# Kernel tuning notes

Hardware: AMD Instinct MI355X
Metric: run time of the kernel (lower is better)

## Reference

```python
import jax, jax.numpy as jnp
from jax import lax
import numpy as np

UNITS = 400
FEAT = 3
B, T = 64, 512


def _lstm_layer(x, Wx, Wh, pi, pf, po, b):
    """Peephole LSTM (Graves 2013). x: [B,T,D] -> [B,T,U]."""
    Bsz = x.shape[0]
    U = Wh.shape[0]
    # Precompute input projections for all timesteps: [B,T,4U]
    xproj = jnp.einsum('btd,dk->btk', x, Wx) + b
    xs = jnp.swapaxes(xproj, 0, 1)  # [T,B,4U]

    def step(carry, xp):
        h, c = carry
        z = xp + h @ Wh  # [B,4U]
        zi, zf, zg, zo = jnp.split(z, 4, axis=-1)
        i = jax.nn.sigmoid(zi + pi * c)
        f = jax.nn.sigmoid(zf + pf * c)
        g = jnp.tanh(zg)
        c_new = f * c + i * g
        o = jax.nn.sigmoid(zo + po * c_new)
        h_new = o * jnp.tanh(c_new)
        return (h_new, c_new), h_new

    init = (jnp.zeros((Bsz, U), x.dtype), jnp.zeros((Bsz, U), x.dtype))
    _, hs = lax.scan(step, init, xs)
    return jnp.swapaxes(hs, 0, 1)  # [B,T,U]


def setup_inputs() -> dict:
    key = jax.random.key(0)
    ks = jax.random.split(key, 32)
    ki = iter(range(32))
    s = 0.05
    d = {'x': jax.random.normal(ks[next(ki)], (B, T, FEAT), jnp.float32)}
    in_dims = [FEAT, UNITS, UNITS]
    for l, din in enumerate(in_dims):
        d[f'Wx{l}'] = jax.random.normal(ks[next(ki)], (din, 4 * UNITS), jnp.float32) * s
        d[f'Wh{l}'] = jax.random.normal(ks[next(ki)], (UNITS, 4 * UNITS), jnp.float32) * s
        d[f'pi{l}'] = jax.random.normal(ks[next(ki)], (UNITS,), jnp.float32) * s
        d[f'pf{l}'] = jax.random.normal(ks[next(ki)], (UNITS,), jnp.float32) * s
        d[f'po{l}'] = jax.random.normal(ks[next(ki)], (UNITS,), jnp.float32) * s
        d[f'b{l}'] = jnp.zeros((4 * UNITS,), jnp.float32)
    d['Wd'] = jax.random.normal(ks[next(ki)], (UNITS, FEAT), jnp.float32) * s
    d['bd'] = jnp.zeros((FEAT,), jnp.float32)
    return d


def reference(x, Wx0, Wh0, pi0, pf0, po0, b0,
              Wx1, Wh1, pi1, pf1, po1, b1,
              Wx2, Wh2, pi2, pf2, po2, b2,
              Wd, bd):
    h = _lstm_layer(x, Wx0, Wh0, pi0, pf0, po0, b0)
    h = _lstm_layer(h, Wx1, Wh1, pi1, pf1, po1, b1)
    h = _lstm_layer(h, Wx2, Wh2, pi2, pf2, po2, b2)
    return h @ Wd + bd  # [B,T,FEAT]
```

## Files before the change

### kernel.cpp

```cpp
#include <hip/hip_runtime.h>
#include <math.h>

#define B64   64
#define TT    512
#define U400  400
#define G1600 1600
#define NBPL  80
#define UPB   5
#define NCOL  (4 * UPB)
#define NW    8
#define NTHR  512
#define NBLK  (3 * NBPL)

__device__ __forceinline__ float ldg_c(const float* p) {
  return __hip_atomic_load(p, __ATOMIC_RELAXED, __HIP_MEMORY_SCOPE_AGENT);
}
__device__ __forceinline__ void stg_c(float* p, float v) {
  __hip_atomic_store(p, v, __ATOMIC_RELAXED, __HIP_MEMORY_SCOPE_AGENT);
}
__device__ __forceinline__ int adl(const unsigned* p) {
  return (int)__hip_atomic_load(p, __ATOMIC_RELAXED, __HIP_MEMORY_SCOPE_AGENT);
}

__global__ void xpose_x_k(const float* __restrict__ x, float* __restrict__ xT) {
  int idx = blockIdx.x * 256 + threadIdx.x;
  if (idx < B64 * TT * 3) {
    int d = idx % 3;
    int t = (idx / 3) % TT;
    int b = idx / (3 * TT);
    xT[(t * 3 + d) * B64 + b] = x[idx];
  }
}

__global__ void transpose_k(const float* __restrict__ in, float* __restrict__ out,
                            int R, int C) {
  __shared__ float tile[32][33];
  int bx = blockIdx.x * 32, by = blockIdx.y * 32;
  int tx = threadIdx.x, ty = threadIdx.y;
  #pragma unroll
  for (int i = ty; i < 32; i += 8) {
    int r = by + i, c = bx + tx;
    if (r < R && c < C) tile[i][tx] = in[(size_t)r * C + c];
  }
  __syncthreads();
  #pragma unroll
  for (int i = ty; i < 32; i += 8) {
    int r = bx + i, c = by + tx;
    if (r < C && c < R) out[(size_t)r * R + c] = tile[tx][i];
  }
}

template <int NQ>
__device__ __forceinline__ void gemm_q(const float* __restrict__ aslab,
                                       int lane,
                                       const float* __restrict__ wg0,
                                       const float* __restrict__ wg1,
                                       const float* __restrict__ wg2,
                                       const float* __restrict__ wg3,
                                       float (&acc)[NCOL]) {
  #pragma unroll 4
  for (int q = 0; q < NQ; ++q) {
    const float a0 = ldg_c(aslab + (size_t)(4 * q + 0) * B64 + lane);
    const float a1 = ldg_c(aslab + (size_t)(4 * q + 1) * B64 + lane);
    const float a2 = ldg_c(aslab + (size_t)(4 * q + 2) * B64 + lane);
    const float a3 = ldg_c(aslab + (size_t)(4 * q + 3) * B64 + lane);
    #pragma unroll
    for (int uu = 0; uu < UPB; ++uu) {
      const float4 w = *reinterpret_cast<const float4*>(wg0 + uu * U400 + 4 * q);
      acc[0 * UPB + uu] += a0 * w.x + a1 * w.y + a2 * w.z + a3 * w.w;
    }
    #pragma unroll
    for (int uu = 0; uu < UPB; ++uu) {
      const float4 w = *reinterpret_cast<const float4*>(wg1 + uu * U400 + 4 * q);
      acc[1 * UPB + uu] += a0 * w.x + a1 * w.y + a2 * w.z + a3 * w.w;
    }
    #pragma unroll
    for (int uu = 0; uu < UPB; ++uu) {
      const float4 w = *reinterpret_cast<const float4*>(wg2 + uu * U400 + 4 * q);
      acc[2 * UPB + uu] += a0 * w.x + a1 * w.y + a2 * w.z + a3 * w.w;
    }
    #pragma unroll
    for (int uu = 0; uu < UPB; ++uu) {
      const float4 w = *reinterpret_cast<const float4*>(wg3 + uu * U400 + 4 * q);
      acc[3 * UPB + uu] += a0 * w.x + a1 * w.y + a2 * w.z + a3 * w.w;
    }
  }
}

struct ScanP {
  const float *xT0, *Wx0;
  const float *WxT1, *WxT2;
  const float *WhT0, *WhT1, *WhT2;
  const float *b0, *b1, *b2;
  const float *pi0, *pi1, *pi2;
  const float *pf0, *pf1, *pf2;
  const float *po0, *po1, *po2;
  float *h0r, *h1r;
  float *h2;
  unsigned *sync;
};

__launch_bounds__(NTHR, 1)
__global__ void lstm_scan_k(ScanP p) {
  const int l    = blockIdx.x / NBPL;
  const int u0   = (blockIdx.x % NBPL) * UPB;
  const int lane = threadIdx.x & 63;
  const int kq   = __builtin_amdgcn_readfirstlane(threadIdx.x >> 6);

  __shared__ float zs[NW][NCOL][B64];

  const float* WhT  = (l == 0) ? p.WhT0 : (l == 1 ? p.WhT1 : p.WhT2);
  const float* WxT  = (l == 1) ? p.WxT1 : p.WxT2;
  const float* bias = (l == 0) ? p.b0  : (l == 1 ? p.b1  : p.b2);
  const float* pi   = (l == 0) ? p.pi0 : (l == 1 ? p.pi1 : p.pi2);
  const float* pf   = (l == 0) ? p.pf0 : (l == 1 ? p.pf1 : p.pf2);
  const float* po   = (l == 0) ? p.po0 : (l == 1 ? p.po1 : p.po2);
  const float* prevb = (l == 1) ? p.h0r : p.h1r;
  float* ownb = (l == 0) ? p.h0r : (l == 1 ? p.h1r : p.h2);
  const int ownmask = (l == 2) ? (TT - 1) : 7;

  unsigned* cnt  = p.sync;
  unsigned* acc_ = p.sync + 3;

  const float* wb; int k0, isH;
  if (l == 0) {
    wb = WhT; isH = 1;
    k0 = (kq < 4) ? kq * 52 : 208 + (kq - 4) * 48;
  } else if (kq < 4) {
    wb = WxT; isH = 0; k0 = kq * 100;
  } else {
    wb = WhT; isH = 1; k0 = (kq - 4) * 100;
  }

  const float* wg0 = wb + (size_t)(0 * U400 + u0) * U400 + k0;
  const float* wg1 = wb + (size_t)(1 * U400 + u0) * U400 + k0;
  const float* wg2 = wb + (size_t)(2 * U400 + u0) * U400 + k0;
  const float* wg3 = wb + (size_t)(3 * U400 + u0) * U400 + k0;

  float creg = 0.f;

  for (int t = 0; t < TT; ++t) {
    if (threadIdx.x == 0) {
      while (adl(&cnt[l]) < t) __builtin_amdgcn_s_sleep(1);
      if (l > 0)
        while (adl(&cnt[l - 1]) < t + 1) __builtin_amdgcn_s_sleep(1);
      if (l < 2)
        while (adl(&cnt[l + 1]) < t - 7) __builtin_amdgcn_s_sleep(1);
    }
    __syncthreads();

    {
      float acc[NCOL];
      #pragma unroll
      for (int c = 0; c < NCOL; ++c) acc[c] = 0.f;

      if (!(isH && t == 0)) {
        const float* aslab = isH
            ? ownb  + (size_t)((t - 1) & ownmask) * (U400 * B64) + (size_t)k0 * B64
            : prevb + (size_t)(t & 7)             * (U400 * B64) + (size_t)k0 * B64;
        if (l == 0) {
          if (kq < 4) gemm_q<13>(aslab, lane, wg0, wg1, wg2, wg3, acc);
          else        gemm_q<12>(aslab, lane, wg0, wg1, wg2, wg3, acc);
        } else {
          gemm_q<25>(aslab, lane, wg0, wg1, wg2, wg3, acc);
        }
      }
      #pragma unroll
      for (int c = 0; c < NCOL; ++c) zs[kq][c][lane] = acc[c];
    }
    __syncthreads();

    if (threadIdx.x < UPB * B64) {
      const int uu = threadIdx.x >> 6;
      const int b  = lane;
      const int u  = u0 + uu;
      float z0 = bias[0 * U400 + u], z1 = bias[1 * U400 + u];
      float z2 = bias[2 * U400 + u], z3 = bias[3 * U400 + u];
      #pragma unroll
      for (int w = 0; w < NW; ++w) {
        z0 += zs[w][0 * UPB + uu][b];
        z1 += zs[w][1 * UPB + uu][b];
        z2 += zs[w][2 * UPB + uu][b];
        z3 += zs[w][3 * UPB + uu][b];
      }
      if (l == 0) {
        #pragma unroll
        for (int dd = 0; dd < 3; ++dd) {
          float xv = p.xT0[(t * 3 + dd) * B64 + b];
          z0 += xv * p.Wx0[dd * G1600 + 0 * U400 + u];
          z1 += xv * p.Wx0[dd * G1600 + 1 * U400 + u];
          z2 += xv * p.Wx0[dd * G1600 + 2 * U400 + u];
          z3 += xv * p.Wx0[dd * G1600 + 3 * U400 + u];
        }
      }
      float cp = creg;
      float ig = 1.f / (1.f + expf(-(z0 + pi[u] * cp)));
      float fg = 1.f / (1.f + expf(-(z1 + pf[u] * cp)));
      float gg = tanhf(z2);
      float cn = fg * cp + ig * gg;
      float og = 1.f / (1.f + expf(-(z3 + po[u] * cn)));
      creg = cn;
      float h = og * tanhf(cn);
      stg_c(&ownb[(size_t)(t & ownmask) * (U400 * B64) + (size_t)u * B64 + b], h);
    }

    __syncthreads();

    if (threadIdx.x == 0) {
      unsigned old = __hip_atomic_fetch_add(&acc_[l], 1u, __ATOMIC_RELAXED,
                                            __HIP_MEMORY_SCOPE_AGENT);
      if (old == (unsigned)((t + 1) * NBPL - 1))
        __hip_atomic_store(&cnt[l], (unsigned)(t + 1), __ATOMIC_RELAXED,
                           __HIP_MEMORY_SCOPE_AGENT);
    }
  }
}

__launch_bounds__(256)
__global__ void dense_k(const float* __restrict__ h2, const float* __restrict__ Wd,
                        const float* __restrict__ bd, float* __restrict__ out) {
  int wid  = blockIdx.x * 4 + (threadIdx.x >> 6);
  int lane = threadIdx.x & 63;
  int t = wid / 3, f = wid - t * 3;
  if (t >= TT) return;
  float acc = bd[f];
  const float* hrow = h2 + (size_t)t * U400 * B64 + lane;
  #pragma unroll 4
  for (int u = 0; u < U400; ++u) acc += hrow[(size_t)u * B64] * Wd[u * 3 + f];
  out[((size_t)lane * TT + t) * 3 + f] = acc;
}

extern "C" void kernel_launch(void* const* d_in, const int* in_sizes, int n_in,
                              void* d_out, int out_size, void* d_ws, size_t ws_size,
                              hipStream_t stream) {
  const float* x   = (const float*)d_in[0];
  const float* Wx0 = (const float*)d_in[1];
  const float* Wh0 = (const float*)d_in[2];
  const float* pi0 = (const float*)d_in[3];
  const float* pf0 = (const float*)d_in[4];
  const float* po0 = (const float*)d_in[5];
  const float* b0  = (const float*)d_in[6];
  const float* Wx1 = (const float*)d_in[7];
  const float* Wh1 = (const float*)d_in[8];
  const float* pi1 = (const float*)d_in[9];
  const float* pf1 = (const float*)d_in[10];
  const float* po1 = (const float*)d_in[11];
  const float* b1  = (const float*)d_in[12];
  const float* Wx2 = (const float*)d_in[13];
  const float* Wh2 = (const float*)d_in[14];
  const float* pi2 = (const float*)d_in[15];
  const float* pf2 = (const float*)d_in[16];
  const float* po2 = (const float*)d_in[17];
  const float* b2  = (const float*)d_in[18];
  const float* Wd  = (const float*)d_in[19];
  const float* bd  = (const float*)d_in[20];

  float* ws   = (float*)d_ws;
  float* xT0  = ws;
  float* WhT0 = xT0  + 98304;
  float* WhT1 = WhT0 + 640000;
  float* WhT2 = WhT1 + 640000;
  float* WxT1 = WhT2 + 640000;
  float* WxT2 = WxT1 + 640000;
  float* h0r  = WxT2 + 640000;
  float* h1r  = h0r  + 204800;
  float* h2   = h1r  + 204800;
  unsigned* syn = (unsigned*)(h2 + 13107200);

  hipMemsetAsync(syn, 0, 64, stream);

  hipLaunchKernelGGL(xpose_x_k, dim3(384), dim3(256), 0, stream, x, xT0);

  dim3 tb(32, 8);
  dim3 tg((G1600 + 31) / 32, (U400 + 31) / 32);
  hipLaunchKernelGGL(transpose_k, tg, tb, 0, stream, Wh0, WhT0, U400, G1600);
  hipLaunchKernelGGL(transpose_k, tg, tb, 0, stream, Wh1, WhT1, U400, G1600);
  hipLaunchKernelGGL(transpose_k, tg, tb, 0, stream, Wh2, WhT2, U400, G1600);
  hipLaunchKernelGGL(transpose_k, tg, tb, 0, stream, Wx1, WxT1, U400, G1600);
  hipLaunchKernelGGL(transpose_k, tg, tb, 0, stream, Wx2, WxT2, U400, G1600);

  ScanP hp;
  hp.xT0 = xT0;  hp.Wx0 = Wx0;
  hp.WxT1 = WxT1; hp.WxT2 = WxT2;
  hp.WhT0 = WhT0; hp.WhT1 = WhT1; hp.WhT2 = WhT2;
  hp.b0 = b0; hp.b1 = b1; hp.b2 = b2;
  hp.pi0 = pi0; hp.pi1 = pi1; hp.pi2 = pi2;
  hp.pf0 = pf0; hp.pf1 = pf1; hp.pf2 = pf2;
  hp.po0 = po0; hp.po1 = po1; hp.po2 = po2;
  hp.h0r = h0r; hp.h1r = h1r; hp.h2 = h2;
  hp.sync = syn;

  void* args[] = { &hp };
  hipLaunchCooperativeKernel((void*)lstm_scan_k, dim3(NBLK), dim3(NTHR),
                             args, 0, stream);

  hipLaunchKernelGGL(dense_k, dim3(384), dim3(256), 0, stream, h2, Wd, bd,
                     (float*)d_out);
}
```

Before: 21.50 ms.

## Split input-projection GEMMs into separate producer blocks and fuse dense head into scan

Layers 1 and 2 previously had each block compute both the Wx·h_prev and Wh·h_self products inside the recurrent critical path. Dedicated blocks now compute the input projections into ring buffers ahead of time, so the recurrent blocks only do the Wh GEMM over all 400 k and add precomputed values. Blocks per layer go from 80 to 50 with 8 units each. The dense output layer becomes one extra block that consumes h2 from an 8-deep ring buffer, which removes the full h2 buffer and the separate kernel launch. Sync counters are padded onto separate cache lines, and a new backpressure edge from the dense block gates layer 2. The cost is more blocks, more inter-block dependencies and an extra global round trip for the projections.

```diff
diff --git a/kernel.cpp b/kernel.cpp
--- a/kernel.cpp
+++ b/kernel.cpp
@@ -5,12 +5,14 @@
 #define TT    512
 #define U400  400
 #define G1600 1600
-#define NBPL  80
-#define UPB   5
+#define NBPL  50
+#define UPB   8
 #define NCOL  (4 * UPB)
 #define NW    8
 #define NTHR  512
-#define NBLK  (3 * NBPL)
+#define NBWH  (3 * NBPL)
+#define NBWX  (2 * NBPL)
+#define NBLK  (NBWH + NBWX + 1)
 
 __device__ __forceinline__ float ldg_c(const float* p) {
   return __hip_atomic_load(p, __ATOMIC_RELAXED, __HIP_MEMORY_SCOPE_AGENT);
@@ -95,42 +97,79 @@
   const float *pi0, *pi1, *pi2;
   const float *pf0, *pf1, *pf2;
   const float *po0, *po1, *po2;
-  float *h0r, *h1r;
-  float *h2;
-  unsigned *sync;
+  const float *Wd, *bd;
+  float *h0r, *h1r, *h2r;
+  float *zx1, *zx2;
+  float *outp;
+  unsigned *syn;
 };
 
-__launch_bounds__(NTHR, 1)
+#define CNT(l)  (p.syn + (l) * 32)
+#define XCNT(l) (p.syn + (3 + (l)) * 32)
+#define DCNT    (p.syn + 6 * 32)
+#define AAC(l)  (p.syn + (7 + (l)) * 32)
+#define XAC(l)  (p.syn + (10 + (l)) * 32)
+
+__launch_bounds__(NTHR)
 __global__ void lstm_scan_k(ScanP p) {
-  const int l    = blockIdx.x / NBPL;
-  const int u0   = (blockIdx.x % NBPL) * UPB;
+  const int bid  = blockIdx.x;
   const int lane = threadIdx.x & 63;
   const int kq   = __builtin_amdgcn_readfirstlane(threadIdx.x >> 6);
+  const int k0   = (kq < 4) ? kq * 52 : 208 + (kq - 4) * 48;
 
   __shared__ float zs[NW][NCOL][B64];
 
-  const float* WhT  = (l == 0) ? p.WhT0 : (l == 1 ? p.WhT1 : p.WhT2);
-  const float* WxT  = (l == 1) ? p.WxT1 : p.WxT2;
+  if (bid == NBWH + NBWX) {
+    for (int t = 0; t < TT; ++t) {
+      if (threadIdx.x == 0)
+        while (adl(CNT(2)) < t + 1) __builtin_amdgcn_s_sleep(1);
+      __syncthreads();
+      {
+        const float* hrow = p.h2r + (size_t)(t & 7) * (U400 * B64) +
+                            (size_t)k0 * B64;
+        const int klen = (kq < 4) ? 52 : 48;
+        float a0 = 0.f, a1 = 0.f, a2 = 0.f;
+        for (int kk = 0; kk < klen; ++kk) {
+          float h = ldg_c(hrow + (size_t)kk * B64 + lane);
+          a0 += h * p.Wd[(k0 + kk) * 3 + 0];
+          a1 += h * p.Wd[(k0 + kk) * 3 + 1];
+          a2 += h * p.Wd[(k0 + kk) * 3 + 2];
+        }
+        zs[kq][0][lane] = a0;
+        zs[kq][1][lane] = a1;
+        zs[kq][2][lane] = a2;
+      }
+      __syncthreads();
+      if (threadIdx.x < 3 * B64) {
+        const int f = threadIdx.x >> 6;
+        float s = p.bd[f];
+        #pragma unroll
+        for (int w = 0; w < NW; ++w) s += zs[w][f][lane];
+        p.outp[((size_t)lane * TT + t) * 3 + f] = s;
+      }
+      __syncthreads();
+      if (threadIdx.x == 0)
+        __hip_atomic_store(DCNT, (unsigned)(t + 1), __ATOMIC_RELAXED,
+                           __HIP_MEMORY_SCOPE_AGENT);
+    }
+    return;
+  }
+
+  const bool wh = (bid < NBWH);
+  const int l   = wh ? (bid / NBPL) : (1 + (bid - NBWH) / NBPL);
+  const int u0  = (wh ? (bid % NBPL) : ((bid - NBWH) % NBPL)) * UPB;
+
   const float* bias = (l == 0) ? p.b0  : (l == 1 ? p.b1  : p.b2);
   const float* pi   = (l == 0) ? p.pi0 : (l == 1 ? p.pi1 : p.pi2);
   const float* pf   = (l == 0) ? p.pf0 : (l == 1 ? p.pf1 : p.pf2);
   const float* po   = (l == 0) ? p.po0 : (l == 1 ? p.po1 : p.po2);
   const float* prevb = (l == 1) ? p.h0r : p.h1r;
-  float* ownb = (l == 0) ? p.h0r : (l == 1 ? p.h1r : p.h2);
-  const int ownmask = (l == 2) ? (TT - 1) : 7;
-
-  unsigned* cnt  = p.sync;
-  unsigned* acc_ = p.sync + 3;
-
-  const float* wb; int k0, isH;
-  if (l == 0) {
-    wb = WhT; isH = 1;
-    k0 = (kq < 4) ? kq * 52 : 208 + (kq - 4) * 48;
-  } else if (kq < 4) {
-    wb = WxT; isH = 0; k0 = kq * 100;
-  } else {
-    wb = WhT; isH = 1; k0 = (kq - 4) * 100;
-  }
+  float* ownb = (l == 0) ? p.h0r : (l == 1 ? p.h1r : p.h2r);
+  float* zxl  = (l == 1) ? p.zx1 : p.zx2;
+
+  const float* wb;
+  if (wh) wb = (l == 0) ? p.WhT0 : (l == 1 ? p.WhT1 : p.WhT2);
+  else    wb = (l == 1) ? p.WxT1 : p.WxT2;
 
   const float* wg0 = wb + (size_t)(0 * U400 + u0) * U400 + k0;
   const float* wg1 = wb + (size_t)(1 * U400 + u0) * U400 + k0;
@@ -141,41 +180,54 @@
 
   for (int t = 0; t < TT; ++t) {
     if (threadIdx.x == 0) {
-      while (adl(&cnt[l]) < t) __builtin_amdgcn_s_sleep(1);
-      if (l > 0)
-        while (adl(&cnt[l - 1]) < t + 1) __builtin_amdgcn_s_sleep(1);
-      if (l < 2)
-        while (adl(&cnt[l + 1]) < t - 7) __builtin_amdgcn_s_sleep(1);
+      if (wh) {
+        while (adl(CNT(l)) < t) __builtin_amdgcn_s_sleep(1);
+        if (l > 0)
+          while (adl(XCNT(l)) < t + 1) __builtin_amdgcn_s_sleep(1);
+        if (l < 2) {
+          while (adl(XCNT(l + 1)) < t - 7) __builtin_amdgcn_s_sleep(1);
+        } else {
+          while (adl(DCNT) < t - 7) __builtin_amdgcn_s_sleep(1);
+        }
+      } else {
+        while (adl(CNT(l - 1)) < t + 1) __builtin_amdgcn_s_sleep(1);
+        while (adl(CNT(l)) < t - 7) __builtin_amdgcn_s_sleep(1);
+      }
     }
     __syncthreads();
+
+    float zq0 = 0.f, zq1 = 0.f, zq2 = 0.f, zq3 = 0.f;
+    if (wh && l > 0) {
+      const int uu = threadIdx.x >> 6;
+      const float* zp = zxl + ((size_t)(t & 7) * G1600 + u0 + uu) * B64 + lane;
+      zq0 = ldg_c(zp + (size_t)(0 * U400) * B64);
+      zq1 = ldg_c(zp + (size_t)(1 * U400) * B64);
+      zq2 = ldg_c(zp + (size_t)(2 * U400) * B64);
+      zq3 = ldg_c(zp + (size_t)(3 * U400) * B64);
+    }
 
     {
       float acc[NCOL];
       #pragma unroll
       for (int c = 0; c < NCOL; ++c) acc[c] = 0.f;
 
-      if (!(isH && t == 0)) {
-        const float* aslab = isH
-            ? ownb  + (size_t)((t - 1) & ownmask) * (U400 * B64) + (size_t)k0 * B64
-            : prevb + (size_t)(t & 7)             * (U400 * B64) + (size_t)k0 * B64;
-        if (l == 0) {
-          if (kq < 4) gemm_q<13>(aslab, lane, wg0, wg1, wg2, wg3, acc);
-          else        gemm_q<12>(aslab, lane, wg0, wg1, wg2, wg3, acc);
-        } else {
-          gemm_q<25>(aslab, lane, wg0, wg1, wg2, wg3, acc);
-        }
+      if (!(wh && t == 0)) {
+        const float* aslab = wh
+            ? ownb  + (size_t)((t - 1) & 7) * (U400 * B64) + (size_t)k0 * B64
+            : prevb + (size_t)(t & 7)       * (U400 * B64) + (size_t)k0 * B64;
+        if (kq < 4) gemm_q<13>(aslab, lane, wg0, wg1, wg2, wg3, acc);
+        else        gemm_q<12>(aslab, lane, wg0, wg1, wg2, wg3, acc);
       }
       #pragma unroll
       for (int c = 0; c < NCOL; ++c) zs[kq][c][lane] = acc[c];
     }
     __syncthreads();
 
-    if (threadIdx.x < UPB * B64) {
+    {
       const int uu = threadIdx.x >> 6;
       const int b  = lane;
       const int u  = u0 + uu;
-      float z0 = bias[0 * U400 + u], z1 = bias[1 * U400 + u];
-      float z2 = bias[2 * U400 + u], z3 = bias[3 * U400 + u];
+      float z0 = 0.f, z1 = 0.f, z2 = 0.f, z3 = 0.f;
       #pragma unroll
       for (int w = 0; w < NW; ++w) {
         z0 += zs[w][0 * UPB + uu][b];
@@ -183,51 +235,52 @@
         z2 += zs[w][2 * UPB + uu][b];
         z3 += zs[w][3 * UPB + uu][b];
       }
-      if (l == 0) {
-        #pragma unroll
-        for (int dd = 0; dd < 3; ++dd) {
-          float xv = p.xT0[(t * 3 + dd) * B64 + b];
-          z0 += xv * p.Wx0[dd * G1600 + 0 * U400 + u];
-          z1 += xv * p.Wx0[dd * G1600 + 1 * U400 + u];
-          z2 += xv * p.Wx0[dd * G1600 + 2 * U400 + u];
-          z3 += xv * p.Wx0[dd * G1600 + 3 * U400 + u];
+      if (wh) {
+        z0 += bias[0 * U400 + u] + zq0;
+        z1 += bias[1 * U400 + u] + zq1;
+        z2 += bias[2 * U400 + u] + zq2;
+        z3 += bias[3 * U400 + u] + zq3;
+        if (l == 0) {
+          #pragma unroll
+          for (int dd = 0; dd < 3; ++dd) {
+            float xv = p.xT0[(t * 3 + dd) * B64 + b];
+            z0 += xv * p.Wx0[dd * G1600 + 0 * U400 + u];
+            z1 += xv * p.Wx0[dd * G1600 + 1 * U400 + u];
+            z2 += xv * p.Wx0[dd * G1600 + 2 * U400 + u];
+            z3 += xv * p.Wx0[dd * G1600 + 3 * U400 + u];
+          }
         }
-      }
-      float cp = creg;
-      float ig = 1.f / (1.f + expf(-(z0 + pi[u] * cp)));
-      float fg = 1.f / (1.f + expf(-(z1 + pf[u] * cp)));
-      float gg = tanhf(z2);
-      float cn = fg * cp + ig * gg;
-      float og = 1.f / (1.f + expf(-(z3 + po[u] * cn)));
-      creg = cn;
-      float h = og * tanhf(cn);
-      stg_c(&ownb[(size_t)(t & ownmask) * (U400 * B64) + (size_t)u * B64 + b], h);
+        float cp = creg;
+        float ig = 1.f / (1.f + expf(-(z0 + pi[u] * cp)));
+        float fg = 1.f / (1.f + expf(-(z1 + pf[u] * cp)));
+        float gg = tanhf(z2);
+        float cn = fg * cp + ig * gg;
+        float og = 1.f / (1.f + expf(-(z3 + po[u] * cn)));
+        creg = cn;
+        float h = og * tanhf(cn);
+        stg_c(&ownb[(size_t)(t & 7) * (U400 * B64) + (size_t)u * B64 + b], h);
+      } else {
+        float* zp = zxl + ((size_t)(t & 7) * G1600 + u0 + uu) * B64 + b;
+        stg_c(zp + (size_t)(0 * U400) * B64, z0);
+        stg_c(zp + (size_t)(1 * U400) * B64, z1);
+        stg_c(zp + (size_t)(2 * U400) * B64, z2);
+        stg_c(zp + (size_t)(3 * U400) * B64, z3);
+      }
     }
 
     __syncthreads();
 
     if (threadIdx.x == 0) {
-      unsigned old = __hip_atomic_fetch_add(&acc_[l], 1u, __ATOMIC_RELAXED,
+      unsigned* ac = wh ? AAC(l) : XAC(l);
+      unsigned old = __hip_atomic_fetch_add(ac, 1u, __ATOMIC_RELAXED,
                                             __HIP_MEMORY_SCOPE_AGENT);
-      if (old == (unsigned)((t + 1) * NBPL - 1))
-        __hip_atomic_store(&cnt[l], (unsigned)(t + 1), __ATOMIC_RELAXED,
+      if (old == (unsigned)((t + 1) * NBPL - 1)) {
+        unsigned* c = wh ? CNT(l) : XCNT(l);
+        __hip_atomic_store(c, (unsigned)(t + 1), __ATOMIC_RELAXED,
                            __HIP_MEMORY_SCOPE_AGENT);
-    }
-  }
-}
-
-__launch_bounds__(256)
-__global__ void dense_k(const float* __restrict__ h2, const float* __restrict__ Wd,
-                        const float* __restrict__ bd, float* __restrict__ out) {
-  int wid  = blockIdx.x * 4 + (threadIdx.x >> 6);
-  int lane = threadIdx.x & 63;
-  int t = wid / 3, f = wid - t * 3;
-  if (t >= TT) return;
-  float acc = bd[f];
-  const float* hrow = h2 + (size_t)t * U400 * B64 + lane;
-  #pragma unroll 4
-  for (int u = 0; u < U400; ++u) acc += hrow[(size_t)u * B64] * Wd[u * 3 + f];
-  out[((size_t)lane * TT + t) * 3 + f] = acc;
+      }
+    }
+  }
 }
 
 extern "C" void kernel_launch(void* const* d_in, const int* in_sizes, int n_in,
@@ -264,10 +317,12 @@
   float* WxT2 = WxT1 + 640000;
   float* h0r  = WxT2 + 640000;
   float* h1r  = h0r  + 204800;
-  float* h2   = h1r  + 204800;
-  unsigned* syn = (unsigned*)(h2 + 13107200);
-
-  hipMemsetAsync(syn, 0, 64, stream);
+  float* h2r  = h1r  + 204800;
+  float* zx1  = h2r  + 204800;
+  float* zx2  = zx1  + 819200;
+  unsigned* syn = (unsigned*)(zx2 + 819200);
+
+  hipMemsetAsync(syn, 0, 13 * 128, stream);
 
   hipLaunchKernelGGL(xpose_x_k, dim3(384), dim3(256), 0, stream, x, xT0);
 
@@ -287,13 +342,13 @@
   hp.pi0 = pi0; hp.pi1 = pi1; hp.pi2 = pi2;
   hp.pf0 = pf0; hp.pf1 = pf1; hp.pf2 = pf2;
   hp.po0 = po0; hp.po1 = po1; hp.po2 = po2;
-  hp.h0r = h0r; hp.h1r = h1r; hp.h2 = h2;
-  hp.sync = syn;
+  hp.Wd = Wd; hp.bd = bd;
+  hp.h0r = h0r; hp.h1r = h1r; hp.h2r = h2r;
+  hp.zx1 = zx1; hp.zx2 = zx2;
+  hp.outp = (float*)d_out;
+  hp.syn = syn;
 
   void* args[] = { &hp };
   hipLaunchCooperativeKernel((void*)lstm_scan_k, dim3(NBLK), dim3(NTHR),
                              args, 0, stream);
-
-  hipLaunchKernelGGL(dense_k, dim3(384), dim3(256), 0, stream, h2, Wd, bd,
-                     (float*)d_out);
-}
+}
```

New measurement: 57.57 ms. 2.68x slower.

## Batch-issue h-slab loads in double buffers and pad sync counters to separate lines

Applied to the files above, without the earlier changes.

Replaces the per-quad load-then-FMA loop in the recurrent GEMM with explicit double-buffered batches of 24-28 coherent loads issued ahead of their consumption. This keeps many loads in flight and hides the global latency of each step's h reads. The sync counters and arrival accumulators are also padded to 128-byte strides so that spinning and atomics on different layers' counters do not share cache lines. The extra buffers raise register pressure.

```diff
diff --git a/kernel.cpp b/kernel.cpp
--- a/kernel.cpp
+++ b/kernel.cpp
@@ -50,38 +50,46 @@
   }
 }
 
-template <int NQ>
-__device__ __forceinline__ void gemm_q(const float* __restrict__ aslab,
-                                       int lane,
-                                       const float* __restrict__ wg0,
-                                       const float* __restrict__ wg1,
-                                       const float* __restrict__ wg2,
-                                       const float* __restrict__ wg3,
-                                       float (&acc)[NCOL]) {
-  #pragma unroll 4
-  for (int q = 0; q < NQ; ++q) {
-    const float a0 = ldg_c(aslab + (size_t)(4 * q + 0) * B64 + lane);
-    const float a1 = ldg_c(aslab + (size_t)(4 * q + 1) * B64 + lane);
-    const float a2 = ldg_c(aslab + (size_t)(4 * q + 2) * B64 + lane);
-    const float a3 = ldg_c(aslab + (size_t)(4 * q + 3) * B64 + lane);
+template <int N>
+__device__ __forceinline__ void issue_n(const float* __restrict__ base, int lane,
+                                        float (&buf)[28]) {
+  #pragma unroll
+  for (int i = 0; i < N; ++i)
+    buf[i] = ldg_c(base + (size_t)i * B64 + lane);
+}
+
+template <int Q>
+__device__ __forceinline__ void consume_q(const float (&buf)[28], int koff,
+                                          const float* __restrict__ wg0,
+                                          const float* __restrict__ wg1,
+                                          const float* __restrict__ wg2,
+                                          const float* __restrict__ wg3,
+                                          float (&acc)[NCOL]) {
+  #pragma unroll
+  for (int q = 0; q < Q; ++q) {
+    const float a0 = buf[4 * q + 0];
+    const float a1 = buf[4 * q + 1];
+    const float a2 = buf[4 * q + 2];
+    const float a3 = buf[4 * q + 3];
+    const int k = koff + 4 * q;
     #pragma unroll
     for (int uu = 0; uu < UPB; ++uu) {
-      const float4 w = *reinterpret_cast<const float4*>(wg0 + uu * U400 + 4 * q);
+      const float4 w = *reinterpret_cast<const float4*>(wg0 + uu * U400 + k);
       acc[0 * UPB + uu] += a0 * w.x + a1 * w.y + a2 * w.z + a3 * w.w;
     }
     #pragma unroll
     for (int uu = 0; uu < UPB; ++uu) {
-      const float4 w = *reinterpret_cast<const float4*>(wg1 + uu * U400 + 4 * q);
+      const float4 w = *reinterpret_cast<const float4*>(wg1 + uu * U400 + k);
       acc[1 * UPB + uu] += a0 * w.x + a1 * w.y + a2 * w.z + a3 * w.w;
     }
     #pragma unroll
     for (int uu = 0; uu < UPB; ++uu) {
-      const float4 w = *reinterpret_cast<const float4*>(wg2 + uu * U400 + 4 * q);
+      const float4 w = *reinterpret_cast<const float4*>(wg2 + uu * U400 + k);
       acc[2 * UPB + uu] += a0 * w.x + a1 * w.y + a2 * w.z + a3 * w.w;
     }
     #pragma unroll
     for (int uu = 0; uu < UPB; ++uu) {
-      const float4 w = *reinterpret_cast<const float4*>(wg3 + uu * U400 + 4 * q);
+      const float4 w = *reinterpret_cast<const float4*>(wg3 + uu * U400 + k);
       acc[3 * UPB + uu] += a0 * w.x + a1 * w.y + a2 * w.z + a3 * w.w;
     }
   }
@@ -97,8 +105,11 @@
   const float *po0, *po1, *po2;
   float *h0r, *h1r;
   float *h2;
-  unsigned *sync;
+  unsigned *syn;
 };
+
+#define CNT(l)  (p.syn + (l) * 32)
+#define AAC(l)  (p.syn + (3 + (l)) * 32)
 
 __launch_bounds__(NTHR, 1)
 __global__ void lstm_scan_k(ScanP p) {
@@ -119,9 +130,6 @@
   float* ownb = (l == 0) ? p.h0r : (l == 1 ? p.h1r : p.h2);
   const int ownmask = (l == 2) ? (TT - 1) : 7;
 
-  unsigned* cnt  = p.sync;
-  unsigned* acc_ = p.sync + 3;
-
   const float* wb; int k0, isH;
   if (l == 0) {
     wb = WhT; isH = 1;
@@ -141,11 +149,11 @@
 
   for (int t = 0; t < TT; ++t) {
     if (threadIdx.x == 0) {
-      while (adl(&cnt[l]) < t) __builtin_amdgcn_s_sleep(1);
+      while (adl(CNT(l)) < t) __builtin_amdgcn_s_sleep(1);
       if (l > 0)
-        while (adl(&cnt[l - 1]) < t + 1) __builtin_amdgcn_s_sleep(1);
+        while (adl(CNT(l - 1)) < t + 1) __builtin_amdgcn_s_sleep(1);
       if (l < 2)
-        while (adl(&cnt[l + 1]) < t - 7) __builtin_amdgcn_s_sleep(1);
+        while (adl(CNT(l + 1)) < t - 7) __builtin_amdgcn_s_sleep(1);
     }
     __syncthreads();
 
@@ -158,11 +166,26 @@
         const float* aslab = isH
             ? ownb  + (size_t)((t - 1) & ownmask) * (U400 * B64) + (size_t)k0 * B64
             : prevb + (size_t)(t & 7)             * (U400 * B64) + (size_t)k0 * B64;
-        if (l == 0) {
-          if (kq < 4) gemm_q<13>(aslab, lane, wg0, wg1, wg2, wg3, acc);
-          else        gemm_q<12>(aslab, lane, wg0, wg1, wg2, wg3, acc);
+        float aA[28], aB[28];
+        if (l != 0) {
+          issue_n<24>(aslab, lane, aA);
+          issue_n<24>(aslab + 24 * B64, lane, aB);
+          consume_q<6>(aA, 0,  wg0, wg1, wg2, wg3, acc);
+          issue_n<24>(aslab + 48 * B64, lane, aA);
+          consume_q<6>(aB, 24, wg0, wg1, wg2, wg3, acc);
+          issue_n<28>(aslab + 72 * B64, lane, aB);
+          consume_q<6>(aA, 48, wg0, wg1, wg2, wg3, acc);
+          consume_q<7>(aB, 72, wg0, wg1, wg2, wg3, acc);
+        } else if (kq < 4) {
+          issue_n<24>(aslab, lane, aA);
+          issue_n<28>(aslab + 24 * B64, lane, aB);
+          consume_q<6>(aA, 0,  wg0, wg1, wg2, wg3, acc);
+          consume_q<7>(aB, 24, wg0, wg1, wg2, wg3, acc);
         } else {
-          gemm_q<25>(aslab, lane, wg0, wg1, wg2, wg3, acc);
+          issue_n<24>(aslab, lane, aA);
+          issue_n<24>(aslab + 24 * B64, lane, aB);
+          consume_q<6>(aA, 0,  wg0, wg1, wg2, wg3, acc);
+          consume_q<6>(aB, 24, wg0, wg1, wg2, wg3, acc);
         }
       }
       #pragma unroll
@@ -207,10 +230,10 @@
     __syncthreads();
 
     if (threadIdx.x == 0) {
-      unsigned old = __hip_atomic_fetch_add(&acc_[l], 1u, __ATOMIC_RELAXED,
+      unsigned old = __hip_atomic_fetch_add(AAC(l), 1u, __ATOMIC_RELAXED,
                                             __HIP_MEMORY_SCOPE_AGENT);
       if (old == (unsigned)((t + 1) * NBPL - 1))
-        __hip_atomic_store(&cnt[l], (unsigned)(t + 1), __ATOMIC_RELAXED,
+        __hip_atomic_store(CNT(l), (unsigned)(t + 1), __ATOMIC_RELAXED,
                            __HIP_MEMORY_SCOPE_AGENT);
     }
   }
@@ -267,7 +290,7 @@
   float* h2   = h1r  + 204800;
   unsigned* syn = (unsigned*)(h2 + 13107200);
 
-  hipMemsetAsync(syn, 0, 64, stream);
+  hipMemsetAsync(syn, 0, 6 * 128, stream);
 
   hipLaunchKernelGGL(xpose_x_k, dim3(384), dim3(256), 0, stream, x, xT0);
 
@@ -288,7 +311,7 @@
   hp.pf0 = pf0; hp.pf1 = pf1; hp.pf2 = pf2;
   hp.po0 = po0; hp.po1 = po1; hp.po2 = po2;
   hp.h0r = h0r; hp.h1r = h1r; hp.h2 = h2;
-  hp.sync = syn;
+  hp.syn = syn;
 
   void* args[] = { &hp };
   hipLaunchCooperativeKernel((void*)lstm_scan_k, dim3(NBLK), dim3(NTHR),
```

After: 34.53 ms. 60.6% more time.
